# Performance work log

Measured on AMD Instinct MI355X. Metric: run time of the kernel, lower is better.

The kernel has to match this reference:

```python
import jax, jax.numpy as jnp
import numpy as np

N = 50000   # nodes
E = 640000  # edges
G = 128     # graphs in batch
H = 128     # hidden_channels
F_NODE, F_EDGE, F_LIG, F_POC = 64, 16, 200, 100
N_STACK = 3  # num_layers - 1


def setup_inputs() -> dict:
    key = jax.random.key(0)
    ks = jax.random.split(key, 24)
    r = lambda i, shape, s=0.05: jax.random.normal(ks[i], shape, dtype=jnp.float32) * s
    z = lambda shape: jnp.zeros(shape, jnp.float32)
    return {
        "x": jax.random.normal(ks[0], (N, F_NODE), dtype=jnp.float32),
        "edge_index": jax.random.randint(ks[1], (2, E), 0, N),
        "edge_attr": jax.random.normal(ks[2], (E, F_EDGE), dtype=jnp.float32),
        "batch": jnp.sort(jax.random.randint(ks[3], (N,), 0, G)),
        "ligand_features": jax.random.normal(ks[4], (G, F_LIG), dtype=jnp.float32),
        "pocket_features": jax.random.normal(ks[5], (G, F_POC), dtype=jnp.float32),
        # conv1 (in != out -> lin_self is a Linear)
        "W1_msg": r(6, (F_NODE, H)), "b1_msg": z((H,)),
        "W1_edge": r(7, (F_EDGE, H)), "b1_edge": z((H,)),
        "W1_self": r(8, (F_NODE, H)), "b1_self": z((H,)),
        # stacked convs (in == out -> lin_self is Identity)
        "Wk_msg": r(9, (N_STACK, H, H)), "bk_msg": z((N_STACK, H)),
        "Wk_edge": r(10, (N_STACK, F_EDGE, H)), "bk_edge": z((N_STACK, H)),
        # global feature / fusion / output heads
        "Wl": r(11, (F_LIG, H)), "bl": z((H,)),
        "Wp": r(12, (F_POC, H)), "bp": z((H,)),
        "Wf": r(13, (3 * H, H)), "bf": z((H,)),
        "Wo": r(14, (H, 1)), "bo": z((1,)),
        "return_embeddings": 0,
    }


def _general_conv(x, edge_index, edge_attr, W_msg, b_msg, W_edge, b_edge, self_out):
    # PyG GeneralConv: msg = lin_msg(x_src) + lin_edge(edge_attr), sum-aggregated at dst,
    # then + lin_self(x) (Identity skip when passed self_out = x).
    src, dst = edge_index[0], edge_index[1]
    edge_term = edge_attr @ W_edge + b_edge            # [E, H] (per-edge, layer-specific)
    msg = x[src] @ W_msg + b_msg + edge_term           # [E, H] gather + GEMM
    agg = jax.ops.segment_sum(msg, dst, num_segments=x.shape[0])  # scatter-add
    return agg + self_out


def reference(x, edge_index, edge_attr, batch, ligand_features, pocket_features,
              W1_msg, b1_msg, W1_edge, b1_edge, W1_self, b1_self,
              Wk_msg, bk_msg, Wk_edge, bk_edge,
              Wl, bl, Wp, bp, Wf, bf, Wo, bo, return_embeddings):
    # conv1 with linear self-connection
    h = _general_conv(x, edge_index, edge_attr, W1_msg, b1_msg, W1_edge, b1_edge,
                      x @ W1_self + b1_self)
    h = jax.nn.relu(h)
    # stacked convs with identity self-connection
    for i in range(N_STACK):
        h = _general_conv(h, edge_index, edge_attr, Wk_msg[i], bk_msg[i],
                          Wk_edge[i], bk_edge[i], h)
        h = jax.nn.relu(h)
    # global mean pool over graphs
    sums = jax.ops.segment_sum(h, batch, num_segments=G)
    counts = jax.ops.segment_sum(jnp.ones((h.shape[0],), h.dtype), batch, num_segments=G)
    pooled = sums / jnp.maximum(counts, 1.0)[:, None]
    # global feature fusion
    lig = ligand_features @ Wl + bl
    poc = pocket_features @ Wp + bp
    fused = jnp.concatenate([pooled, lig, poc], axis=1) @ Wf + bf
    # dropout is a no-op in eval mode
    if not return_embeddings:
        fused = fused @ Wo + bo
    return fused
```

## Files before the change

### kernel.cpp

```cpp
#include <hip/hip_runtime.h>
#include <cstdint>

#define NN 50000
#define NE 640000
#define NG 128
#define HD 128
#define FN 64
#define FE 16
#define FL 200
#define FPOC 100
#define NSTACK 3
#define NBUK 196

typedef unsigned short ushort_t;
typedef short short8 __attribute__((ext_vector_type(8)));
typedef float f32x4 __attribute__((ext_vector_type(4)));

__device__ __forceinline__ ushort_t f2bf(float f) {
    unsigned u = __float_as_uint(f);
    unsigned r = (u + 0x7fffu + ((u >> 16) & 1u)) >> 16;
    return (ushort_t)r;
}
__device__ __forceinline__ float bf2f(ushort_t u) {
    return __uint_as_float(((unsigned)u) << 16);
}


__global__ void hist_kernel(const int* __restrict__ ei, int* __restrict__ bucket_cnt) {
    __shared__ int l[NBUK];
    int t = threadIdx.x;
    if (t < NBUK) l[t] = 0;
    __syncthreads();
    int base = blockIdx.x * 2048;
#pragma unroll
    for (int i = 0; i < 8; ++i) {
        int e = base + i * 256 + t;
        if (e < NE) atomicAdd(&l[ei[NE + e] >> 8], 1);
    }
    __syncthreads();
    if (t < NBUK && l[t]) atomicAdd(&bucket_cnt[t], l[t]);
}

__global__ void scan_kernel(const int* __restrict__ bucket_cnt,
                            int* __restrict__ bucket_base, int* __restrict__ bucket_cur) {
    __shared__ int s[256];
    int t = threadIdx.x;
    int v = (t < NBUK) ? bucket_cnt[t] : 0;
    s[t] = v;
    __syncthreads();
    for (int off = 1; off < 256; off <<= 1) {
        int w = (t >= off) ? s[t - off] : 0;
        __syncthreads();
        s[t] += w;
        __syncthreads();
    }
    if (t < NBUK) {
        int b = s[t] - v;
        bucket_base[t] = b;
        bucket_cur[t] = b;
    }
}

__global__ __launch_bounds__(256) void scatter_bin(const int* __restrict__ ei,
                                                   int* __restrict__ bucket_cur,
                                                   int2* __restrict__ staging) {
    __shared__ int lcnt[NBUK];
    __shared__ int lrun[NBUK];
    int t = threadIdx.x;
    if (t < NBUK) lcnt[t] = 0;
    __syncthreads();
    int base = blockIdx.x * 4096;
#pragma unroll
    for (int i = 0; i < 16; ++i) {
        int e = base + i * 256 + t;
        if (e < NE) atomicAdd(&lcnt[ei[NE + e] >> 8], 1);
    }
    __syncthreads();
    if (t < NBUK) {
        int c = lcnt[t];
        lrun[t] = c ? atomicAdd(&bucket_cur[t], c) : 0;
        lcnt[t] = 0;
    }
    __syncthreads();
#pragma unroll
    for (int i = 0; i < 16; ++i) {
        int e = base + i * 256 + t;
        if (e < NE) {
            int s = ei[e];
            int d = ei[NE + e];
            int bk = d >> 8;
            int off = atomicAdd(&lcnt[bk], 1);
            staging[lrun[bk] + off] = make_int2(s, e | ((d & 255) << 20));
        }
    }
}

__global__ __launch_bounds__(256) void place_kernel(
    const int* __restrict__ bucket_base, const int* __restrict__ bucket_cnt,
    const int2* __restrict__ staging, int* __restrict__ row_beg,
    int* __restrict__ cnt, int2* __restrict__ csr) {
    __shared__ int hist[256];
    __shared__ int curp[256];
    int t = threadIdx.x;
    int b = blockIdx.x;
    int n0 = b << 8;
    hist[t] = 0;
    __syncthreads();
    int ebase = bucket_base[b];
    int ecnt = bucket_cnt[b];
    for (int i = t; i < ecnt; i += 256) atomicAdd(&hist[staging[ebase + i].y >> 20], 1);
    __syncthreads();
    int v = hist[t];
    __syncthreads();
    for (int off = 1; off < 256; off <<= 1) {
        int w = (t >= off) ? hist[t - off] : 0;
        __syncthreads();
        hist[t] += w;
        __syncthreads();
    }
    int rb = ebase + hist[t] - v;
    if (n0 + t < NN) {
        row_beg[n0 + t] = rb;
        cnt[n0 + t] = v;
    }
    curp[t] = rb;
    __syncthreads();
    for (int i = t; i < ecnt; i += 256) {
        int2 p = staging[ebase + i];
        int dl = p.y >> 20;
        int e = p.y & 0xFFFFF;
        int pos = atomicAdd(&curp[dl], 1);
        csr[pos] = make_int2(p.x, e);
    }
}

__global__ __launch_bounds__(256) void sege_kernel(
    const int* __restrict__ row_beg, const int* __restrict__ cnt,
    const int2* __restrict__ csr, const float* __restrict__ ea,
    ushort_t* __restrict__ segaug) {
    int node = blockIdx.x * 4 + (threadIdx.x >> 6);
    if (node >= NN) return;
    int lane = threadIdx.x & 63;
    int G = lane >> 2, q4 = (lane & 3) * 4;
    int beg = row_beg[node];
    int dg = cnt[node];
    int end = beg + dg;
    float4 a = make_float4(0.f, 0.f, 0.f, 0.f);
    for (int j = beg + G; j < end; j += 16) {
        int e = csr[j].y;
        float4 v = *(const float4*)(ea + (size_t)e * FE + q4);
        a.x += v.x; a.y += v.y; a.z += v.z; a.w += v.w;
    }
    for (int m = 4; m <= 32; m <<= 1) {
        a.x += __shfl_xor(a.x, m);
        a.y += __shfl_xor(a.y, m);
        a.z += __shfl_xor(a.z, m);
        a.w += __shfl_xor(a.w, m);
    }
    if (lane < 4) {
        ushort_t o[4] = {f2bf(a.x), f2bf(a.y), f2bf(a.z), f2bf(a.w)};
        *(uint2*)(segaug + (size_t)node * 32 + lane * 4) = *(uint2*)o;
    } else if (lane < 8) {
        ushort_t o[4] = {0, 0, 0, 0};
        if (lane == 4) { o[0] = f2bf((float)dg); o[1] = f2bf(1.f); }
        *(uint2*)(segaug + (size_t)node * 32 + lane * 4) = *(uint2*)o;
    }
}


__global__ void repack_kernel(const float* __restrict__ W1_msg,
                              const float* __restrict__ W1_self,
                              const float* __restrict__ W1_edge,
                              const float* __restrict__ b1_msg,
                              const float* __restrict__ b1_edge,
                              const float* __restrict__ b1_self,
                              const float* __restrict__ Wk_msg,
                              const float* __restrict__ Wk_edge,
                              const float* __restrict__ bk_msg,
                              const float* __restrict__ bk_edge,
                              ushort_t* __restrict__ pack) {
    int mid = blockIdx.y;
    const float *W = nullptr, *bm = nullptr, *be = nullptr, *bc = nullptr;
    int K;
    size_t doff;
    bool aug = false;
    if (mid == 0)      { W = W1_msg;  K = 64;  doff = 0; }
    else if (mid == 1) { W = W1_self; K = 64;  doff = 8192; }
    else if (mid == 2) { W = W1_edge; bm = b1_msg; be = b1_edge; bc = b1_self;
                         K = 32; doff = 16384; aug = true; }
    else if (mid <= 5) { int i = mid - 3; W = Wk_msg + (size_t)i * HD * HD;
                         K = 128; doff = 20480 + (size_t)i * 16384; }
    else               { int i = mid - 6; W = Wk_edge + (size_t)i * FE * HD;
                         bm = bk_msg + i * HD; be = bk_edge + i * HD;
                         K = 32; doff = 69632 + (size_t)i * 4096; aug = true; }
    int KS = K / 32;
    int t = blockIdx.x * 256 + threadIdx.x;
    if (t >= 8 * KS * 64) return;
    int lane = t & 63;
    int nk = t >> 6;
    int ks = nk % KS, nt = nk / KS;
    int n = nt * 16 + (lane & 15);
    int kb = ks * 32 + (lane >> 4) * 8;
    ushort_t o[8];
#pragma unroll
    for (int j = 0; j < 8; ++j) {
        int k = kb + j;
        float v;
        if (!aug)         v = W[(size_t)k * HD + n];
        else if (k < 16)  v = W[(size_t)k * HD + n];
        else if (k == 16) v = bm[n] + be[n];
        else if (k == 17) v = bc ? bc[n] : 0.f;
        else              v = 0.f;
        o[j] = f2bf(v);
    }
    *(uint4*)(pack + doff + (size_t)t * 8) = *(uint4*)o;
}


__global__ __launch_bounds__(256) void gemm_mfma_conv1(const float* __restrict__ A,
                                                       const ushort_t* __restrict__ segaug,
                                                       const ushort_t* __restrict__ pack,
                                                       ushort_t* __restrict__ Cm,
                                                       ushort_t* __restrict__ Cs, int n) {
    constexpr int STR = 72, SSTR = 40;
    __shared__ __align__(16) ushort_t As[64 * STR];
    __shared__ __align__(16) ushort_t Ss[64 * SSTR];
    int tid = threadIdx.x;
    int row0 = blockIdx.x * 64;
#pragma unroll
    for (int p = 0; p < 2; ++p) {
        int c = p * 256 + tid;
        int r = c >> 3, col = (c & 7) * 8;
        int gr = row0 + r;
        float4 f0 = make_float4(0.f, 0.f, 0.f, 0.f), f1 = f0;
        if (gr < n) {
            f0 = *(const float4*)(A + (size_t)gr * FN + col);
            f1 = *(const float4*)(A + (size_t)gr * FN + col + 4);
        }
        ushort_t o[8] = {f2bf(f0.x), f2bf(f0.y), f2bf(f0.z), f2bf(f0.w),
                         f2bf(f1.x), f2bf(f1.y), f2bf(f1.z), f2bf(f1.w)};
        *(uint4*)(&As[r * STR + col]) = *(uint4*)o;
    }
    {
        int c = tid;
        int r = c >> 2, col = (c & 3) * 8;
        int gr = row0 + r;
        uint4 v = make_uint4(0u, 0u, 0u, 0u);
        if (gr < n) v = *(const uint4*)(segaug + (size_t)gr * 32 + col);
        *(uint4*)(&Ss[r * SSTR + col]) = v;
    }
    __syncthreads();
    int lane = tid & 63, wave = tid >> 6;
    int m = lane & 15, quad = lane >> 4;
    f32x4 acc[16];
#pragma unroll
    for (int i = 0; i < 16; ++i) acc[i] = (f32x4)(0.f);
    const short8* Bmsg = (const short8*)pack;
    const short8* Bself = (const short8*)(pack + 8192);
    const short8* Beaug = (const short8*)(pack + 16384);
#pragma unroll
    for (int ks = 0; ks < 2; ++ks) {
        short8 a = *(const short8*)(&As[(wave * 16 + m) * STR + ks * 32 + quad * 8]);
#pragma unroll
        for (int nt = 0; nt < 8; ++nt) {
            acc[nt] = __builtin_amdgcn_mfma_f32_16x16x32_bf16(
                a, Bmsg[(nt * 2 + ks) * 64 + lane], acc[nt], 0, 0, 0);
            acc[8 + nt] = __builtin_amdgcn_mfma_f32_16x16x32_bf16(
                a, Bself[(nt * 2 + ks) * 64 + lane], acc[8 + nt], 0, 0, 0);
        }
    }
    {
        short8 sa = *(const short8*)(&Ss[(wave * 16 + m) * SSTR + quad * 8]);
#pragma unroll
        for (int nt = 0; nt < 8; ++nt)
            acc[8 + nt] = __builtin_amdgcn_mfma_f32_16x16x32_bf16(
                sa, Beaug[nt * 64 + lane], acc[8 + nt], 0, 0, 0);
    }
#pragma unroll
    for (int nt = 0; nt < 8; ++nt) {
        int col = nt * 16 + m;
#pragma unroll
        for (int r = 0; r < 4; ++r) {
            int grow = row0 + wave * 16 + quad * 4 + r;
            if (grow < n) {
                Cm[(size_t)grow * HD + col] = f2bf(acc[nt][r]);
                Cs[(size_t)grow * HD + col] = f2bf(acc[8 + nt][r]);
            }
        }
    }
}


__device__ __forceinline__ void accum8(float* a, uint4 v) {
    a[0] += __uint_as_float(v.x << 16);
    a[1] += __uint_as_float(v.x & 0xffff0000u);
    a[2] += __uint_as_float(v.y << 16);
    a[3] += __uint_as_float(v.y & 0xffff0000u);
    a[4] += __uint_as_float(v.z << 16);
    a[5] += __uint_as_float(v.z & 0xffff0000u);
    a[6] += __uint_as_float(v.w << 16);
    a[7] += __uint_as_float(v.w & 0xffff0000u);
}

__global__ __launch_bounds__(256, 6) void fused_agg_gemm(
    const int* __restrict__ row_beg, const int* __restrict__ cnt,
    const int2* __restrict__ csr, const ushort_t* __restrict__ msg_in,
    const ushort_t* __restrict__ S_in, const ushort_t* __restrict__ segaug,
    const ushort_t* __restrict__ Bm, const ushort_t* __restrict__ Be,
    ushort_t* __restrict__ msg_out, ushort_t* __restrict__ S_out) {
    constexpr int STR = 136, SSTR = 40;
    __shared__ __align__(16) ushort_t Hs[16 * STR];
    __shared__ __align__(16) ushort_t Ss[16 * SSTR];
    int tid = threadIdx.x;
    int node0 = blockIdx.x * 16;
    if (tid < 64) {
        int r = tid >> 2, col = (tid & 3) * 8;
        *(uint4*)(&Ss[r * SSTR + col]) =
            *(const uint4*)(segaug + (size_t)(node0 + r) * 32 + col);
    }
    int nl = tid >> 4;
    int node = node0 + nl;
    int c8 = (tid & 15) * 8;
    int beg = row_beg[node];
    int end = beg + cnt[node];
    float a0[8] = {0.f, 0.f, 0.f, 0.f, 0.f, 0.f, 0.f, 0.f};
    float a1[8] = {0.f, 0.f, 0.f, 0.f, 0.f, 0.f, 0.f, 0.f};
    int j = beg;
    for (; j + 3 < end; j += 4) {
        int u0 = csr[j].x, u1 = csr[j + 1].x, u2 = csr[j + 2].x, u3 = csr[j + 3].x;
        uint4 v0 = *(const uint4*)(msg_in + (size_t)u0 * HD + c8);
        uint4 v1 = *(const uint4*)(msg_in + (size_t)u1 * HD + c8);
        uint4 v2 = *(const uint4*)(msg_in + (size_t)u2 * HD + c8);
        uint4 v3 = *(const uint4*)(msg_in + (size_t)u3 * HD + c8);
        accum8(a0, v0);
        accum8(a1, v1);
        accum8(a0, v2);
        accum8(a1, v3);
    }
    for (; j < end; ++j) {
        uint4 v = *(const uint4*)(msg_in + (size_t)csr[j].x * HD + c8);
        accum8(a0, v);
    }
    accum8(a0, *(const uint4*)(S_in + (size_t)node * HD + c8));
    {
        ushort_t h8[8];
#pragma unroll
        for (int i = 0; i < 8; ++i) h8[i] = f2bf(fmaxf(a0[i] + a1[i], 0.f));
        *(uint4*)(&Hs[nl * STR + c8]) = *(uint4*)h8;
    }
    __syncthreads();
    int lane = tid & 63, wave = tid >> 6;
    int m = lane & 15, quad = lane >> 4;
    f32x4 acc[2], accE[2];
#pragma unroll
    for (int t = 0; t < 2; ++t) { acc[t] = (f32x4)(0.f); accE[t] = (f32x4)(0.f); }
    const short8* Bmv = (const short8*)Bm;
    const short8* Bev = (const short8*)Be;
#pragma unroll
    for (int ks = 0; ks < 4; ++ks) {
        short8 a = *(const short8*)(&Hs[m * STR + ks * 32 + quad * 8]);
#pragma unroll
        for (int t = 0; t < 2; ++t) {
            int nt = wave * 2 + t;
            acc[t] = __builtin_amdgcn_mfma_f32_16x16x32_bf16(
                a, Bmv[(nt * 4 + ks) * 64 + lane], acc[t], 0, 0, 0);
        }
    }
    {
        short8 sa = *(const short8*)(&Ss[m * SSTR + quad * 8]);
#pragma unroll
        for (int t = 0; t < 2; ++t) {
            int nt = wave * 2 + t;
            accE[t] = __builtin_amdgcn_mfma_f32_16x16x32_bf16(
                sa, Bev[nt * 64 + lane], accE[t], 0, 0, 0);
        }
    }
#pragma unroll
    for (int t = 0; t < 2; ++t) {
        int col = (wave * 2 + t) * 16 + m;
#pragma unroll
        for (int r = 0; r < 4; ++r) {
            int rl = quad * 4 + r;
            size_t gidx = (size_t)(node0 + rl) * HD + col;
            msg_out[gidx] = f2bf(acc[t][r]);
            S_out[gidx] = f2bf(accE[t][r] + bf2f(Hs[rl * STR + col]));
        }
    }
}


__global__ __launch_bounds__(256, 6) void agg_pool_kernel(
    const int* __restrict__ row_beg, const int* __restrict__ cnt,
    const int2* __restrict__ csr, const ushort_t* __restrict__ xm,
    const ushort_t* __restrict__ selfb, const int* __restrict__ batch,
    float* __restrict__ pooled) {
    __shared__ float hloc[16][HD];
    int tid = threadIdx.x;
    int node0 = blockIdx.x * 16;
    int nl = tid >> 4;
    int node = node0 + nl;
    int c8 = (tid & 15) * 8;
    int beg = row_beg[node];
    int end = beg + cnt[node];
    float a0[8] = {0.f, 0.f, 0.f, 0.f, 0.f, 0.f, 0.f, 0.f};
    float a1[8] = {0.f, 0.f, 0.f, 0.f, 0.f, 0.f, 0.f, 0.f};
    int j = beg;
    for (; j + 3 < end; j += 4) {
        int u0 = csr[j].x, u1 = csr[j + 1].x, u2 = csr[j + 2].x, u3 = csr[j + 3].x;
        uint4 v0 = *(const uint4*)(xm + (size_t)u0 * HD + c8);
        uint4 v1 = *(const uint4*)(xm + (size_t)u1 * HD + c8);
        uint4 v2 = *(const uint4*)(xm + (size_t)u2 * HD + c8);
        uint4 v3 = *(const uint4*)(xm + (size_t)u3 * HD + c8);
        accum8(a0, v0);
        accum8(a1, v1);
        accum8(a0, v2);
        accum8(a1, v3);
    }
    for (; j < end; ++j) {
        uint4 v = *(const uint4*)(xm + (size_t)csr[j].x * HD + c8);
        accum8(a0, v);
    }
    accum8(a0, *(const uint4*)(selfb + (size_t)node * HD + c8));
#pragma unroll
    for (int i = 0; i < 8; ++i) hloc[nl][c8 + i] = fmaxf(a0[i] + a1[i], 0.f);
    __syncthreads();
    if (tid < HD) {
        int f = tid;
        float run = 0.f;
        int gprev = batch[node0];
        for (int r = 0; r < 16; ++r) {
            int g = batch[node0 + r];
            if (g != gprev) {
                atomicAdd(&pooled[gprev * HD + f], run);
                run = 0.f;
                gprev = g;
            }
            run += hloc[r][f];
        }
        atomicAdd(&pooled[gprev * HD + f], run);
    }
}


__global__ void head_kernel(const float* __restrict__ pooled, const int* __restrict__ batch,
                            const float* __restrict__ lf, const float* __restrict__ pfe,
                            const float* __restrict__ Wl, const float* __restrict__ bl,
                            const float* __restrict__ Wp, const float* __restrict__ bp,
                            const float* __restrict__ Wf, const float* __restrict__ bfv,
                            const float* __restrict__ Wo, const float* __restrict__ bo,
                            float* __restrict__ out) {
    __shared__ float cat[3 * HD];
    __shared__ float red[HD];
    int g = blockIdx.x, j = threadIdx.x;
    int lo = 0, hi = NN;
    while (lo < hi) { int m = (lo + hi) >> 1; if (batch[m] < g) lo = m + 1; else hi = m; }
    int s0 = lo;
    lo = s0; hi = NN;
    while (lo < hi) { int m = (lo + hi) >> 1; if (batch[m] < g + 1) lo = m + 1; else hi = m; }
    float cntf = (float)(lo - s0);
    cat[j] = pooled[(size_t)g * HD + j] / fmaxf(cntf, 1.f);
    float s = bl[j];
    for (int k = 0; k < FL; ++k) s += lf[g * FL + k] * Wl[k * HD + j];
    cat[HD + j] = s;
    s = bp[j];
    for (int k = 0; k < FPOC; ++k) s += pfe[g * FPOC + k] * Wp[k * HD + j];
    cat[2 * HD + j] = s;
    __syncthreads();
    float fj = bfv[j];
    for (int k = 0; k < 3 * HD; ++k) fj += cat[k] * Wf[k * HD + j];
    red[j] = fj * Wo[j];
    __syncthreads();
    for (int off = 64; off > 0; off >>= 1) {
        if (j < off) red[j] += red[j + off];
        __syncthreads();
    }
    if (j == 0) out[g] = red[0] + bo[0];
}


extern "C" void kernel_launch(void* const* d_in, const int* in_sizes, int n_in,
                              void* d_out, int out_size, void* d_ws, size_t ws_size,
                              hipStream_t stream) {
    const float* x       = (const float*)d_in[0];
    const int*   ei      = (const int*)d_in[1];
    const float* ea      = (const float*)d_in[2];
    const int*   batch   = (const int*)d_in[3];
    const float* lf      = (const float*)d_in[4];
    const float* pfe     = (const float*)d_in[5];
    const float* W1_msg  = (const float*)d_in[6];
    const float* b1_msg  = (const float*)d_in[7];
    const float* W1_edge = (const float*)d_in[8];
    const float* b1_edge = (const float*)d_in[9];
    const float* W1_self = (const float*)d_in[10];
    const float* b1_self = (const float*)d_in[11];
    const float* Wk_msg  = (const float*)d_in[12];
    const float* bk_msg  = (const float*)d_in[13];
    const float* Wk_edge = (const float*)d_in[14];
    const float* bk_edge = (const float*)d_in[15];
    const float* Wl      = (const float*)d_in[16];
    const float* bl      = (const float*)d_in[17];
    const float* Wp      = (const float*)d_in[18];
    const float* bp      = (const float*)d_in[19];
    const float* Wf      = (const float*)d_in[20];
    const float* bfv     = (const float*)d_in[21];
    const float* Wo      = (const float*)d_in[22];
    const float* bo      = (const float*)d_in[23];

    char* wsp = (char*)d_ws;
    size_t off = 0;
    auto carve = [&](size_t bytes) -> void* {
        char* p = wsp + off;
        off += (bytes + 255) & ~(size_t)255;
        return (void*)p;
    };
    int*      bucket_cnt  = (int*)carve((size_t)NBUK * 4);
    float*    pooled      = (float*)carve((size_t)NG * HD * 4);
    int*      bucket_base = (int*)carve((size_t)NBUK * 4);
    int*      bucket_cur  = (int*)carve((size_t)NBUK * 4);
    int*      row_beg     = (int*)carve((size_t)NN * 4);
    int*      cnt         = (int*)carve((size_t)NN * 4);
    int2*     staging     = (int2*)carve((size_t)NE * 8);
    int2*     csr         = (int2*)carve((size_t)NE * 8);
    ushort_t* segaug      = (ushort_t*)carve((size_t)NN * 32 * 2);
    ushort_t* pack        = (ushort_t*)carve((size_t)81920 * 2);
    ushort_t* bufC        = (ushort_t*)carve((size_t)NN * HD * 2);
    ushort_t* bufD        = (ushort_t*)carve((size_t)NN * HD * 2);
    ushort_t* bufS        = (ushort_t*)carve((size_t)NN * HD * 2);
    ushort_t* bufT        = (ushort_t*)carve((size_t)NN * HD * 2);

    size_t clr = (size_t)((char*)(pooled + NG * HD) - (char*)bucket_cnt);
    hipMemsetAsync(bucket_cnt, 0, clr, stream);

    hist_kernel<<<(NE + 2047) / 2048, 256, 0, stream>>>(ei, bucket_cnt);
    scan_kernel<<<1, 256, 0, stream>>>(bucket_cnt, bucket_base, bucket_cur);
    scatter_bin<<<(NE + 4095) / 4096, 256, 0, stream>>>(ei, bucket_cur, staging);
    place_kernel<<<NBUK, 256, 0, stream>>>(bucket_base, bucket_cnt, staging, row_beg,
                                           cnt, csr);
    sege_kernel<<<(NN + 3) / 4, 256, 0, stream>>>(row_beg, cnt, csr, ea, segaug);
    repack_kernel<<<dim3(8, 9), 256, 0, stream>>>(W1_msg, W1_self, W1_edge, b1_msg,
                                                  b1_edge, b1_self, Wk_msg, Wk_edge,
                                                  bk_msg, bk_edge, pack);

    gemm_mfma_conv1<<<dim3((NN + 63) / 64), 256, 0, stream>>>(x, segaug, pack, bufC,
                                                              bufS, NN);
    fused_agg_gemm<<<NN / 16, 256, 0, stream>>>(row_beg, cnt, csr, bufC, bufS, segaug,
                                                pack + 20480, pack + 69632, bufD, bufT);
    fused_agg_gemm<<<NN / 16, 256, 0, stream>>>(row_beg, cnt, csr, bufD, bufT, segaug,
                                                pack + 20480 + 16384, pack + 69632 + 4096,
                                                bufC, bufS);
    fused_agg_gemm<<<NN / 16, 256, 0, stream>>>(row_beg, cnt, csr, bufC, bufS, segaug,
                                                pack + 20480 + 32768, pack + 69632 + 8192,
                                                bufD, bufT);
    agg_pool_kernel<<<NN / 16, 256, 0, stream>>>(row_beg, cnt, csr, bufD, bufT, batch,
                                                 pooled);

    head_kernel<<<NG, HD, 0, stream>>>(pooled, batch, lf, pfe, Wl, bl, Wp, bp, Wf, bfv,
                                       Wo, bo, (float*)d_out);
}
```

Measured before the change: 356.8 us.

## Balance edge aggregation across block with shared-memory atomics and split CSR arrays

Edge aggregation in the fused conv and pool kernels no longer gives each 16-thread group one destination node. The block's contiguous edge range is split evenly across the 16 groups, with software-prefetched gathers. Partial sums go into a shared fp32 tile through LDS atomicAdd whenever the destination changes, which removes load imbalance from uneven node degrees. The CSR is split into a packed source+local-dst array and a separate edge-id array, and row_beg gains a sentinel entry in place of the cnt array. The cost is LDS atomics, an extra shared tile and extra barriers, and each group now issues one gather at a time instead of four.

Measured after the change: 540.7 us. 1.52x slower.

```diff
diff --git a/kernel.cpp b/kernel.cpp
--- a/kernel.cpp
+++ b/kernel.cpp
@@ -98,7 +98,7 @@
 __global__ __launch_bounds__(256) void place_kernel(
     const int* __restrict__ bucket_base, const int* __restrict__ bucket_cnt,
     const int2* __restrict__ staging, int* __restrict__ row_beg,
-    int* __restrict__ cnt, int2* __restrict__ csr) {
+    int* __restrict__ csrc, int* __restrict__ cedge) {
     __shared__ int hist[256];
     __shared__ int curp[256];
     int t = threadIdx.x;
@@ -119,10 +119,8 @@
         __syncthreads();
     }
     int rb = ebase + hist[t] - v;
-    if (n0 + t < NN) {
-        row_beg[n0 + t] = rb;
-        cnt[n0 + t] = v;
-    }
+    if (n0 + t < NN) row_beg[n0 + t] = rb;
+    if (b == 0 && t == 0) row_beg[NN] = NE;
     curp[t] = rb;
     __syncthreads();
     for (int i = t; i < ecnt; i += 256) {
@@ -130,24 +128,23 @@
         int dl = p.y >> 20;
         int e = p.y & 0xFFFFF;
         int pos = atomicAdd(&curp[dl], 1);
-        csr[pos] = make_int2(p.x, e);
+        csrc[pos] = p.x | ((dl & 15) << 20);
+        cedge[pos] = e;
     }
 }
 
 __global__ __launch_bounds__(256) void sege_kernel(
-    const int* __restrict__ row_beg, const int* __restrict__ cnt,
-    const int2* __restrict__ csr, const float* __restrict__ ea,
-    ushort_t* __restrict__ segaug) {
+    const int* __restrict__ row_beg, const int* __restrict__ cedge,
+    const float* __restrict__ ea, ushort_t* __restrict__ segaug) {
     int node = blockIdx.x * 4 + (threadIdx.x >> 6);
     if (node >= NN) return;
     int lane = threadIdx.x & 63;
     int G = lane >> 2, q4 = (lane & 3) * 4;
-    int beg = row_beg[node];
-    int dg = cnt[node];
-    int end = beg + dg;
+    int beg = row_beg[node], end = row_beg[node + 1];
+    int dg = end - beg;
     float4 a = make_float4(0.f, 0.f, 0.f, 0.f);
     for (int j = beg + G; j < end; j += 16) {
-        int e = csr[j].y;
+        int e = cedge[j];
         float4 v = *(const float4*)(ea + (size_t)e * FE + q4);
         a.x += v.x; a.y += v.y; a.z += v.z; a.w += v.w;
     }
@@ -302,15 +299,60 @@
     a[7] += __uint_as_float(v.w & 0xffff0000u);
 }
 
+#define HP (HD + 4)
+
+#define EDGE_AGG(hloc)                                                           \
+    {                                                                            \
+        int qw = tid >> 4;                                                       \
+        int epq = (nE + 15) >> 4;                                                \
+        int j = b0 + qw * epq;                                                   \
+        int qend = b0 + nE;                                                      \
+        if (j + epq < qend) qend = j + epq;                                      \
+        float a0[8] = {0.f, 0.f, 0.f, 0.f, 0.f, 0.f, 0.f, 0.f};                  \
+        int dlcur = -1;                                                          \
+        int pn = 0;                                                              \
+        uint4 vn = make_uint4(0u, 0u, 0u, 0u);                                   \
+        if (j < qend) {                                                          \
+            pn = csrc[j];                                                        \
+            vn = *(const uint4*)(msg_in + (size_t)(pn & 0xFFFFF) * HD + c8);     \
+        }                                                                        \
+        while (j < qend) {                                                       \
+            int p = pn;                                                          \
+            uint4 v = vn;                                                        \
+            ++j;                                                                 \
+            if (j < qend) {                                                      \
+                pn = csrc[j];                                                    \
+                vn = *(const uint4*)(msg_in + (size_t)(pn & 0xFFFFF) * HD + c8); \
+            }                                                                    \
+            int dl = p >> 20;                                                    \
+            if (dl != dlcur) {                                                   \
+                if (dlcur >= 0) {                                                \
+                    float* dst = &hloc[dlcur * HP + c8];                         \
+                    _Pragma("unroll") for (int i = 0; i < 8; ++i)                \
+                        atomicAdd(dst + i, a0[i]);                               \
+                }                                                                \
+                _Pragma("unroll") for (int i = 0; i < 8; ++i) a0[i] = 0.f;       \
+                dlcur = dl;                                                      \
+            }                                                                    \
+            accum8(a0, v);                                                       \
+        }                                                                        \
+        if (dlcur >= 0) {                                                        \
+            float* dst = &hloc[dlcur * HP + c8];                                 \
+            _Pragma("unroll") for (int i = 0; i < 8; ++i)                        \
+                atomicAdd(dst + i, a0[i]);                                       \
+        }                                                                        \
+    }
+
 __global__ __launch_bounds__(256, 6) void fused_agg_gemm(
-    const int* __restrict__ row_beg, const int* __restrict__ cnt,
-    const int2* __restrict__ csr, const ushort_t* __restrict__ msg_in,
-    const ushort_t* __restrict__ S_in, const ushort_t* __restrict__ segaug,
-    const ushort_t* __restrict__ Bm, const ushort_t* __restrict__ Be,
-    ushort_t* __restrict__ msg_out, ushort_t* __restrict__ S_out) {
+    const int* __restrict__ row_beg, const int* __restrict__ csrc,
+    const ushort_t* __restrict__ msg_in, const ushort_t* __restrict__ S_in,
+    const ushort_t* __restrict__ segaug, const ushort_t* __restrict__ Bm,
+    const ushort_t* __restrict__ Be, ushort_t* __restrict__ msg_out,
+    ushort_t* __restrict__ S_out) {
     constexpr int STR = 136, SSTR = 40;
     __shared__ __align__(16) ushort_t Hs[16 * STR];
     __shared__ __align__(16) ushort_t Ss[16 * SSTR];
+    __shared__ __align__(16) float hloc[16 * HP];
     int tid = threadIdx.x;
     int node0 = blockIdx.x * 16;
     if (tid < 64) {
@@ -318,34 +360,22 @@
         *(uint4*)(&Ss[r * SSTR + col]) =
             *(const uint4*)(segaug + (size_t)(node0 + r) * 32 + col);
     }
+#pragma unroll
+    for (int i = tid; i < 16 * HP; i += 256) hloc[i] = 0.f;
+    int b0 = row_beg[node0];
+    int nE = row_beg[node0 + 16] - b0;
+    int c8 = (tid & 15) * 8;
+    __syncthreads();
+    EDGE_AGG(hloc)
+    __syncthreads();
     int nl = tid >> 4;
-    int node = node0 + nl;
-    int c8 = (tid & 15) * 8;
-    int beg = row_beg[node];
-    int end = beg + cnt[node];
-    float a0[8] = {0.f, 0.f, 0.f, 0.f, 0.f, 0.f, 0.f, 0.f};
-    float a1[8] = {0.f, 0.f, 0.f, 0.f, 0.f, 0.f, 0.f, 0.f};
-    int j = beg;
-    for (; j + 3 < end; j += 4) {
-        int u0 = csr[j].x, u1 = csr[j + 1].x, u2 = csr[j + 2].x, u3 = csr[j + 3].x;
-        uint4 v0 = *(const uint4*)(msg_in + (size_t)u0 * HD + c8);
-        uint4 v1 = *(const uint4*)(msg_in + (size_t)u1 * HD + c8);
-        uint4 v2 = *(const uint4*)(msg_in + (size_t)u2 * HD + c8);
-        uint4 v3 = *(const uint4*)(msg_in + (size_t)u3 * HD + c8);
-        accum8(a0, v0);
-        accum8(a1, v1);
-        accum8(a0, v2);
-        accum8(a1, v3);
-    }
-    for (; j < end; ++j) {
-        uint4 v = *(const uint4*)(msg_in + (size_t)csr[j].x * HD + c8);
-        accum8(a0, v);
-    }
-    accum8(a0, *(const uint4*)(S_in + (size_t)node * HD + c8));
     {
+        float s[8] = {0.f, 0.f, 0.f, 0.f, 0.f, 0.f, 0.f, 0.f};
+        accum8(s, *(const uint4*)(S_in + (size_t)(node0 + nl) * HD + c8));
         ushort_t h8[8];
 #pragma unroll
-        for (int i = 0; i < 8; ++i) h8[i] = f2bf(fmaxf(a0[i] + a1[i], 0.f));
+        for (int i = 0; i < 8; ++i)
+            h8[i] = f2bf(fmaxf(hloc[nl * HP + c8 + i] + s[i], 0.f));
         *(uint4*)(&Hs[nl * STR + c8]) = *(uint4*)h8;
     }
     __syncthreads();
@@ -390,39 +420,28 @@
 
 
 __global__ __launch_bounds__(256, 6) void agg_pool_kernel(
-    const int* __restrict__ row_beg, const int* __restrict__ cnt,
-    const int2* __restrict__ csr, const ushort_t* __restrict__ xm,
-    const ushort_t* __restrict__ selfb, const int* __restrict__ batch,
-    float* __restrict__ pooled) {
-    __shared__ float hloc[16][HD];
+    const int* __restrict__ row_beg, const int* __restrict__ csrc,
+    const ushort_t* __restrict__ msg_in, const ushort_t* __restrict__ selfb,
+    const int* __restrict__ batch, float* __restrict__ pooled) {
+    __shared__ __align__(16) float hloc[16 * HP];
     int tid = threadIdx.x;
     int node0 = blockIdx.x * 16;
+#pragma unroll
+    for (int i = tid; i < 16 * HP; i += 256) hloc[i] = 0.f;
+    int b0 = row_beg[node0];
+    int nE = row_beg[node0 + 16] - b0;
+    int c8 = (tid & 15) * 8;
+    __syncthreads();
+    EDGE_AGG(hloc)
+    __syncthreads();
     int nl = tid >> 4;
-    int node = node0 + nl;
-    int c8 = (tid & 15) * 8;
-    int beg = row_beg[node];
-    int end = beg + cnt[node];
-    float a0[8] = {0.f, 0.f, 0.f, 0.f, 0.f, 0.f, 0.f, 0.f};
-    float a1[8] = {0.f, 0.f, 0.f, 0.f, 0.f, 0.f, 0.f, 0.f};
-    int j = beg;
-    for (; j + 3 < end; j += 4) {
-        int u0 = csr[j].x, u1 = csr[j + 1].x, u2 = csr[j + 2].x, u3 = csr[j + 3].x;
-        uint4 v0 = *(const uint4*)(xm + (size_t)u0 * HD + c8);
-        uint4 v1 = *(const uint4*)(xm + (size_t)u1 * HD + c8);
-        uint4 v2 = *(const uint4*)(xm + (size_t)u2 * HD + c8);
-        uint4 v3 = *(const uint4*)(xm + (size_t)u3 * HD + c8);
-        accum8(a0, v0);
-        accum8(a1, v1);
-        accum8(a0, v2);
-        accum8(a1, v3);
-    }
-    for (; j < end; ++j) {
-        uint4 v = *(const uint4*)(xm + (size_t)csr[j].x * HD + c8);
-        accum8(a0, v);
-    }
-    accum8(a0, *(const uint4*)(selfb + (size_t)node * HD + c8));
-#pragma unroll
-    for (int i = 0; i < 8; ++i) hloc[nl][c8 + i] = fmaxf(a0[i] + a1[i], 0.f);
+    {
+        float s[8] = {0.f, 0.f, 0.f, 0.f, 0.f, 0.f, 0.f, 0.f};
+        accum8(s, *(const uint4*)(selfb + (size_t)(node0 + nl) * HD + c8));
+#pragma unroll
+        for (int i = 0; i < 8; ++i)
+            hloc[nl * HP + c8 + i] = fmaxf(hloc[nl * HP + c8 + i] + s[i], 0.f);
+    }
     __syncthreads();
     if (tid < HD) {
         int f = tid;
@@ -435,7 +454,7 @@
                 run = 0.f;
                 gprev = g;
             }
-            run += hloc[r][f];
+            run += hloc[r * HP + f];
         }
         atomicAdd(&pooled[gprev * HD + f], run);
     }
@@ -517,10 +536,10 @@
     float*    pooled      = (float*)carve((size_t)NG * HD * 4);
     int*      bucket_base = (int*)carve((size_t)NBUK * 4);
     int*      bucket_cur  = (int*)carve((size_t)NBUK * 4);
-    int*      row_beg     = (int*)carve((size_t)NN * 4);
-    int*      cnt         = (int*)carve((size_t)NN * 4);
+    int*      row_beg     = (int*)carve((size_t)(NN + 1) * 4);
     int2*     staging     = (int2*)carve((size_t)NE * 8);
-    int2*     csr         = (int2*)carve((size_t)NE * 8);
+    int*      csrc        = (int*)carve((size_t)NE * 4);
+    int*      cedge       = (int*)carve((size_t)NE * 4);
     ushort_t* segaug      = (ushort_t*)carve((size_t)NN * 32 * 2);
     ushort_t* pack        = (ushort_t*)carve((size_t)81920 * 2);
     ushort_t* bufC        = (ushort_t*)carve((size_t)NN * HD * 2);
@@ -535,23 +554,23 @@
     scan_kernel<<<1, 256, 0, stream>>>(bucket_cnt, bucket_base, bucket_cur);
     scatter_bin<<<(NE + 4095) / 4096, 256, 0, stream>>>(ei, bucket_cur, staging);
     place_kernel<<<NBUK, 256, 0, stream>>>(bucket_base, bucket_cnt, staging, row_beg,
-                                           cnt, csr);
-    sege_kernel<<<(NN + 3) / 4, 256, 0, stream>>>(row_beg, cnt, csr, ea, segaug);
+                                           csrc, cedge);
+    sege_kernel<<<(NN + 3) / 4, 256, 0, stream>>>(row_beg, cedge, ea, segaug);
     repack_kernel<<<dim3(8, 9), 256, 0, stream>>>(W1_msg, W1_self, W1_edge, b1_msg,
                                                   b1_edge, b1_self, Wk_msg, Wk_edge,
                                                   bk_msg, bk_edge, pack);
 
     gemm_mfma_conv1<<<dim3((NN + 63) / 64), 256, 0, stream>>>(x, segaug, pack, bufC,
                                                               bufS, NN);
-    fused_agg_gemm<<<NN / 16, 256, 0, stream>>>(row_beg, cnt, csr, bufC, bufS, segaug,
+    fused_agg_gemm<<<NN / 16, 256, 0, stream>>>(row_beg, csrc, bufC, bufS, segaug,
                                                 pack + 20480, pack + 69632, bufD, bufT);
-    fused_agg_gemm<<<NN / 16, 256, 0, stream>>>(row_beg, cnt, csr, bufD, bufT, segaug,
+    fused_agg_gemm<<<NN / 16, 256, 0, stream>>>(row_beg, csrc, bufD, bufT, segaug,
                                                 pack + 20480 + 16384, pack + 69632 + 4096,
                                                 bufC, bufS);
-    fused_agg_gemm<<<NN / 16, 256, 0, stream>>>(row_beg, cnt, csr, bufC, bufS, segaug,
+    fused_agg_gemm<<<NN / 16, 256, 0, stream>>>(row_beg, csrc, bufC, bufS, segaug,
                                                 pack + 20480 + 32768, pack + 69632 + 8192,
                                                 bufD, bufT);
-    agg_pool_kernel<<<NN / 16, 256, 0, stream>>>(row_beg, cnt, csr, bufD, bufT, batch,
+    agg_pool_kernel<<<NN / 16, 256, 0, stream>>>(row_beg, csrc, bufD, bufT, batch,
                                                  pooled);
 
     head_kernel<<<NG, HD, 0, stream>>>(pooled, batch, lf, pfe, Wl, bl, Wp, bp, Wf, bfv,
```
